# Optimization experiments

Hardware: AMD Instinct MI355X
Metric: run time of the kernel (lower is better)

The kernel has to match this reference:

```python
import jax, jax.numpy as jnp
import numpy as np

N, E, F, H, DE, C, G = 50000, 800000, 128, 128, 16, 2, 32
NEG_SLOPE = 0.2

def setup_inputs() -> dict:
    key = jax.random.key(0)
    ks = jax.random.split(key, 13)
    s = 0.05  # small init scale for weights
    return {
        "x": jax.random.normal(ks[0], (N, F), jnp.float32),
        "edge_index": jax.random.randint(ks[1], (2, E), 0, N, dtype=jnp.int32),
        "edge_attr": jax.random.normal(ks[2], (E, DE), jnp.float32),
        "batch": jnp.sort(jax.random.randint(ks[3], (N,), 0, G, dtype=jnp.int32)),
        "Wl": jax.random.normal(ks[4], (F, H), jnp.float32) * s,
        "bl": jnp.zeros((H,), jnp.float32),
        "Wr": jax.random.normal(ks[5], (F, H), jnp.float32) * s,
        "br": jnp.zeros((H,), jnp.float32),
        "We": jax.random.normal(ks[6], (DE, H), jnp.float32) * s,
        "att": jax.random.normal(ks[7], (H,), jnp.float32) * s,
        "bias_conv": jnp.zeros((H,), jnp.float32),
        "Wc": jax.random.normal(ks[8], (H, C), jnp.float32) * s,
        "bc": jnp.zeros((C,), jnp.float32),
    }

def reference(x, edge_index, edge_attr, batch, Wl, bl, Wr, br, We, att, bias_conv, Wc, bc):
    n = x.shape[0]
    src, dst = edge_index[0], edge_index[1]
    # add self loops; self-loop edge_attr = mean of incoming edge_attr (PyG fill_value='mean')
    ones_e = jnp.ones((edge_attr.shape[0],), x.dtype)
    deg = jax.ops.segment_sum(ones_e, dst, num_segments=n)
    loop_attr = jax.ops.segment_sum(edge_attr, dst, num_segments=n) / jnp.maximum(deg, 1.0)[:, None]
    idx = jnp.arange(n, dtype=src.dtype)
    src2 = jnp.concatenate([src, idx])
    dst2 = jnp.concatenate([dst, idx])
    ea2 = jnp.concatenate([edge_attr, loop_attr], axis=0)  # [E+N, DE]
    # GATv2: separate source/target transforms
    xl = x @ Wl + bl          # [N, H] (source / message features)
    xr = x @ Wr + br          # [N, H] (target features)
    e = ea2 @ We              # [E+N, H]
    m = xl[src2] + xr[dst2] + e                      # per-edge features
    logit = jax.nn.leaky_relu(m, NEG_SLOPE) @ att    # [E+N]
    # segment softmax over destination nodes (every node has a self loop)
    mx = jax.ops.segment_max(logit, dst2, num_segments=n)
    ex = jnp.exp(logit - mx[dst2])
    den = jax.ops.segment_sum(ex, dst2, num_segments=n)
    alpha = ex / den[dst2]
    out = jax.ops.segment_sum(alpha[:, None] * xl[src2], dst2, num_segments=n) + bias_conv
    h = jax.nn.relu(out)
    # global mean pool over graphs (eval mode: dropout is identity)
    cnt = jax.ops.segment_sum(jnp.ones((n,), x.dtype), batch, num_segments=G)
    pooled = jax.ops.segment_sum(h, batch, num_segments=G) / jnp.maximum(cnt, 1.0)[:, None]
    return pooled @ Wc + bc
```

## Files before the change

kernel.cpp:

```cpp
#include <hip/hip_runtime.h>

#define FDIM 128
#define HDIM 128
#define DE   16
#define GG   32
#define CAP  48
#define NPB  4
#define EA_STRIDE 20
#define NEG_SLOPE 0.2f

__device__ __forceinline__ float2 f2fma(float a, float2 b, float2 c) {
    float2 r; r.x = fmaf(a, b.x, c.x); r.y = fmaf(a, b.y, c.y); return r;
}

__global__ void k_scatter(const int* __restrict__ src, const int* __restrict__ dst,
                          int* __restrict__ cursor, int2* __restrict__ list, int E) {
    int i = blockIdx.x * blockDim.x + threadIdx.x;
    if (i < E) {
        int d = dst[i];
        int p = atomicAdd(&cursor[d], 1);
        if (p < CAP - 1) list[d * CAP + p] = make_int2(src[i], i);
    }
}

__global__ __launch_bounds__(256) void k_gemm(
    const float* __restrict__ x,
    const float* __restrict__ Wl, const float* __restrict__ bl,
    const float* __restrict__ Wr, const float* __restrict__ br,
    float* __restrict__ xl, float* __restrict__ xr, int M,
    int* __restrict__ cursor, float* __restrict__ pool, int* __restrict__ cnt)
{
    __shared__ float As[32][65];

    const int tid = threadIdx.x;
    for (int i = blockIdx.x * 256 + tid; i < M; i += gridDim.x * 256) cursor[i] = 0;
    if (blockIdx.x == 0) {
        for (int i = tid; i < GG * HDIM; i += 256) pool[i] = 0.f;
        if (tid < GG) cnt[tid] = 0;
    }
    const int r0 = blockIdx.x * 64;
    const int tx = tid & 31, ty = tid >> 5;
    float acc[8][8] = {};

    for (int kc = 0; kc < FDIM; kc += 32) {
        #pragma unroll
        for (int vv = 0; vv < 2; ++vv) {
            int v = tid + vv * 256;
            int mrow = v >> 3, kq = v & 7;
            int r = r0 + mrow; r = (r < M) ? r : (M - 1);
            float4 xv = *reinterpret_cast<const float4*>(&x[(size_t)r * FDIM + kc + kq * 4]);
            As[kq * 4 + 0][mrow] = xv.x;
            As[kq * 4 + 1][mrow] = xv.y;
            As[kq * 4 + 2][mrow] = xv.z;
            As[kq * 4 + 3][mrow] = xv.w;
        }
        __syncthreads();
        #pragma unroll
        for (int k = 0; k < 32; ++k) {
            float4 b0 = *reinterpret_cast<const float4*>(&Wl[(size_t)(kc + k) * HDIM + tx * 4]);
            float4 b1 = *reinterpret_cast<const float4*>(&Wr[(size_t)(kc + k) * HDIM + tx * 4]);
            float4 a0 = *reinterpret_cast<const float4*>(&As[k][ty * 8]);
            float4 a1 = *reinterpret_cast<const float4*>(&As[k][ty * 8 + 4]);
            float a8[8] = {a0.x, a0.y, a0.z, a0.w, a1.x, a1.y, a1.z, a1.w};
            #pragma unroll
            for (int i = 0; i < 8; ++i) {
                acc[i][0] = fmaf(a8[i], b0.x, acc[i][0]);
                acc[i][1] = fmaf(a8[i], b0.y, acc[i][1]);
                acc[i][2] = fmaf(a8[i], b0.z, acc[i][2]);
                acc[i][3] = fmaf(a8[i], b0.w, acc[i][3]);
                acc[i][4] = fmaf(a8[i], b1.x, acc[i][4]);
                acc[i][5] = fmaf(a8[i], b1.y, acc[i][5]);
                acc[i][6] = fmaf(a8[i], b1.z, acc[i][6]);
                acc[i][7] = fmaf(a8[i], b1.w, acc[i][7]);
            }
        }
        __syncthreads();
    }
    float4 bvl = *reinterpret_cast<const float4*>(&bl[tx * 4]);
    float4 bvr = *reinterpret_cast<const float4*>(&br[tx * 4]);
    #pragma unroll
    for (int i = 0; i < 8; ++i) {
        int r = r0 + ty * 8 + i;
        if (r < M) {
            float4 ol, orr;
            ol.x  = acc[i][0] + bvl.x; ol.y  = acc[i][1] + bvl.y;
            ol.z  = acc[i][2] + bvl.z; ol.w  = acc[i][3] + bvl.w;
            orr.x = acc[i][4] + bvr.x; orr.y = acc[i][5] + bvr.y;
            orr.z = acc[i][6] + bvr.z; orr.w = acc[i][7] + bvr.w;
            *reinterpret_cast<float4*>(&xl[(size_t)r * HDIM + tx * 4]) = ol;
            *reinterpret_cast<float4*>(&xr[(size_t)r * HDIM + tx * 4]) = orr;
        }
    }
}

__global__ __launch_bounds__(256, 4) void k_node(
    const float* __restrict__ xl, const float* __restrict__ xr,
    const float* __restrict__ edge_attr, const float* __restrict__ We,
    const float* __restrict__ att, const float* __restrict__ bias_conv,
    const int* __restrict__ deg, const int2* __restrict__ list,
    float* __restrict__ hN, int n0base, int N)
{
    __shared__ float ea_s[NPB][CAP][EA_STRIDE];

    const int tid  = threadIdx.x;
    const int lane = tid & 63;
    const int w    = tid >> 6;
    const int n    = n0base + blockIdx.x * NPB + w;
    if (n >= N) return;

    const float2 at2 = *reinterpret_cast<const float2*>(&att[2 * lane]);
    const float2 xr2 = *reinterpret_cast<const float2*>(&xr[(size_t)n * HDIM + 2 * lane]);
    float2 Wreg[DE];
    #pragma unroll
    for (int k = 0; k < DE; ++k)
        Wreg[k] = *reinterpret_cast<const float2*>(&We[k * HDIM + 2 * lane]);

    const int dfull  = deg[n];
    const int dcap   = dfull < (CAP - 1) ? dfull : (CAP - 1);
    const int cnt    = dcap + 1;
    const int nb     = (cnt + 7) >> 3;
    const int padcnt = nb * 8;

    if (lane < dcap) {
        int2 se = list[(size_t)n * CAP + lane];
        const float4* ep = reinterpret_cast<const float4*>(&edge_attr[(size_t)se.y * DE]);
        float4 v0 = ep[0], v1 = ep[1], v2 = ep[2], v3 = ep[3];
        float* row = &ea_s[w][lane][0];
        *reinterpret_cast<float4*>(row + 0)  = v0;
        *reinterpret_cast<float4*>(row + 4)  = v1;
        *reinterpret_cast<float4*>(row + 8)  = v2;
        *reinterpret_cast<float4*>(row + 12) = v3;
        row[16] = __int_as_float(se.x);
    } else if (lane < padcnt) {
        ea_s[w][lane][16] = __int_as_float(n);
    }
    asm volatile("s_waitcnt lgkmcnt(0)" ::: "memory");

    float2 A[8], B[8];
    int sA[8], sB[8];

    auto loadS = [&](int* s, int b) {
        #pragma unroll
        for (int jj = 0; jj < 8; ++jj)
            s[jj] = __float_as_int(ea_s[w][b * 8 + jj][16]);
    };
    auto issue = [&](float2* R, const int* s) {
        #pragma unroll
        for (int jj = 0; jj < 8; ++jj)
            R[jj] = *reinterpret_cast<const float2*>(&xl[(size_t)s[jj] * HDIM + 2 * lane]);
    };

    loadS(sA, 0);
    issue(A, sA);

    {
        const int k = lane & 15, q = lane >> 4;
        float s = 0.f;
        for (int j = q; j < dcap; j += 4) s += ea_s[w][j][k];
        s += __shfl_xor(s, 16);
        s += __shfl_xor(s, 32);
        if (q == 0) ea_s[w][dcap][k] = s / (float)(dfull > 1 ? dfull : 1);
    }
    asm volatile("s_waitcnt lgkmcnt(0)" ::: "memory");

    float m = -1e30f, d = 0.f;
    float2 o = make_float2(0.f, 0.f);

    auto compute = [&](float2* R, int b) {
        const int j0 = b * 8;
        float p[8];
        #pragma unroll
        for (int jj = 0; jj < 8; ++jj) {
            const float* ear = &ea_s[w][j0 + jj][0];
            float4 e0 = *reinterpret_cast<const float4*>(ear + 0);
            float4 e1 = *reinterpret_cast<const float4*>(ear + 4);
            float4 e2 = *reinterpret_cast<const float4*>(ear + 8);
            float4 e3 = *reinterpret_cast<const float4*>(ear + 12);
            float2 s = xr2;
            s = f2fma(e0.x, Wreg[0],  s);
            s = f2fma(e0.y, Wreg[1],  s);
            s = f2fma(e0.z, Wreg[2],  s);
            s = f2fma(e0.w, Wreg[3],  s);
            s = f2fma(e1.x, Wreg[4],  s);
            s = f2fma(e1.y, Wreg[5],  s);
            s = f2fma(e1.z, Wreg[6],  s);
            s = f2fma(e1.w, Wreg[7],  s);
            s = f2fma(e2.x, Wreg[8],  s);
            s = f2fma(e2.y, Wreg[9],  s);
            s = f2fma(e2.z, Wreg[10], s);
            s = f2fma(e2.w, Wreg[11], s);
            s = f2fma(e3.x, Wreg[12], s);
            s = f2fma(e3.y, Wreg[13], s);
            s = f2fma(e3.z, Wreg[14], s);
            s = f2fma(e3.w, Wreg[15], s);
            s.x += R[jj].x;
            s.y += R[jj].y;
            s.x = s.x > 0.f ? s.x : NEG_SLOPE * s.x;
            s.y = s.y > 0.f ? s.y : NEG_SLOPE * s.y;
            p[jj] = fmaf(s.x, at2.x, s.y * at2.y);
        }
        {
            float sd0 = (lane & 1) ? p[0] : p[4];
            float sd1 = (lane & 1) ? p[1] : p[5];
            float sd2 = (lane & 1) ? p[2] : p[6];
            float sd3 = (lane & 1) ? p[3] : p[7];
            float r0 = __shfl_xor(sd0, 1), r1 = __shfl_xor(sd1, 1);
            float r2 = __shfl_xor(sd2, 1), r3 = __shfl_xor(sd3, 1);
            p[0] = ((lane & 1) ? p[4] : p[0]) + r0;
            p[1] = ((lane & 1) ? p[5] : p[1]) + r1;
            p[2] = ((lane & 1) ? p[6] : p[2]) + r2;
            p[3] = ((lane & 1) ? p[7] : p[3]) + r3;
        }
        {
            float sd0 = (lane & 2) ? p[0] : p[2];
            float sd1 = (lane & 2) ? p[1] : p[3];
            float r0 = __shfl_xor(sd0, 2), r1 = __shfl_xor(sd1, 2);
            p[0] = ((lane & 2) ? p[2] : p[0]) + r0;
            p[1] = ((lane & 2) ? p[3] : p[1]) + r1;
        }
        {
            float sd = (lane & 4) ? p[0] : p[1];
            float r = __shfl_xor(sd, 4);
            p[0] = ((lane & 4) ? p[1] : p[0]) + r;
        }
        float t = p[0];
        t += __shfl_xor(t, 8);
        t += __shfl_xor(t, 16);
        t += __shfl_xor(t, 32);
        if (lane < 8) {
            int e = ((lane & 1) << 2) | (lane & 2) | ((lane >> 2) & 1);
            ea_s[w][e][17] = t;
        }
        asm volatile("s_waitcnt lgkmcnt(0)" ::: "memory");
        float tt[8];
        #pragma unroll
        for (int jj = 0; jj < 8; ++jj) tt[jj] = ea_s[w][jj][17];

        const int bk = cnt - j0;
        float mx = m;
        #pragma unroll
        for (int jj = 0; jj < 8; ++jj) {
            if (jj >= bk) tt[jj] = -1e30f;
            mx = fmaxf(mx, tt[jj]);
        }
        const float sc = __expf(m - mx);
        float pj[8], psum = 0.f;
        #pragma unroll
        for (int jj = 0; jj < 8; ++jj) { pj[jj] = __expf(tt[jj] - mx); psum += pj[jj]; }
        d = fmaf(d, sc, psum);
        float2 acc = make_float2(0.f, 0.f);
        #pragma unroll
        for (int jj = 0; jj < 8; ++jj) acc = f2fma(pj[jj], R[jj], acc);
        o.x = fmaf(o.x, sc, acc.x);
        o.y = fmaf(o.y, sc, acc.y);
        m = mx;
    };

    for (int b = 0; b < nb; ++b) {
        const bool odd = (b & 1) != 0;
        if (b + 1 < nb) {
            if (odd) { loadS(sA, b + 1); issue(A, sA); }
            else     { loadS(sB, b + 1); issue(B, sB); }
        }
        if (odd) compute(B, b); else compute(A, b);
    }

    const float inv = 1.f / d;
    const float2 bc2 = *reinterpret_cast<const float2*>(&bias_conv[2 * lane]);
    float2 res;
    res.x = fmaxf(fmaf(o.x, inv, bc2.x), 0.f);
    res.y = fmaxf(fmaf(o.y, inv, bc2.y), 0.f);
    *reinterpret_cast<float2*>(&hN[(size_t)n * HDIM + 2 * lane]) = res;
}

__global__ __launch_bounds__(128) void k_pool(
    const float* __restrict__ hN, const int* __restrict__ batch,
    float* __restrict__ pool, int* __restrict__ cnt, int N)
{
    const int t  = threadIdx.x;
    const int n0 = blockIdx.x * 32;
    if (n0 >= N) return;
    const int n1 = (n0 + 32 < N) ? (n0 + 32) : N;
    const int gfirst = batch[n0];
    const int glast  = batch[n1 - 1];
    if (gfirst == glast) {
        float acc = 0.f;
        #pragma unroll 8
        for (int nn = n0; nn < n1; ++nn) acc += hN[(size_t)nn * HDIM + t];
        atomicAdd(&pool[gfirst * HDIM + t], acc);
        if (t == 0) atomicAdd(&cnt[gfirst], n1 - n0);
        return;
    }
    int curg = gfirst;
    float acc = 0.f;
    int c = 0;
    for (int nn = n0; nn < n1; ++nn) {
        int g = batch[nn];
        if (g != curg) {
            atomicAdd(&pool[curg * HDIM + t], acc);
            if (t == 0) atomicAdd(&cnt[curg], c);
            acc = 0.f; c = 0; curg = g;
        }
        acc += hN[(size_t)nn * HDIM + t];
        ++c;
    }
    atomicAdd(&pool[curg * HDIM + t], acc);
    if (t == 0) atomicAdd(&cnt[curg], c);
}

__global__ void k_final(const float* __restrict__ pool, const int* __restrict__ cnt,
                        const float* __restrict__ Wc, const float* __restrict__ bc,
                        float* __restrict__ out)
{
    int t = threadIdx.x;
    if (t < GG * 2) {
        int g = t >> 1, c = t & 1;
        float inv = 1.f / (float)(cnt[g] > 1 ? cnt[g] : 1);
        float s = 0.f;
        #pragma unroll 16
        for (int h = 0; h < HDIM; ++h) s += pool[g * HDIM + h] * Wc[h * 2 + c];
        out[t] = s * inv + bc[c];
    }
}

extern "C" void kernel_launch(void* const* d_in, const int* in_sizes, int n_in,
                              void* d_out, int out_size, void* d_ws, size_t ws_size,
                              hipStream_t stream) {
    const float* x         = (const float*)d_in[0];
    const int*   ei        = (const int*)  d_in[1];
    const float* edge_attr = (const float*)d_in[2];
    const int*   batch     = (const int*)  d_in[3];
    const float* Wl        = (const float*)d_in[4];
    const float* bl        = (const float*)d_in[5];
    const float* Wr        = (const float*)d_in[6];
    const float* br        = (const float*)d_in[7];
    const float* We        = (const float*)d_in[8];
    const float* att       = (const float*)d_in[9];
    const float* bias_conv = (const float*)d_in[10];
    const float* Wc        = (const float*)d_in[11];
    const float* bc        = (const float*)d_in[12];
    float* out = (float*)d_out;

    const int N = in_sizes[0] / FDIM;
    const int E = in_sizes[1] / 2;
    const int* srcp = ei;
    const int* dstp = ei + E;

    char* ws = (char*)d_ws;
    size_t off = 0;
    auto alloc = [&](size_t bytes) { char* p = ws + off; off = (off + bytes + 255) & ~(size_t)255; return p; };
    int*   cursor = (int*)  alloc((size_t)N * 4);
    int2*  list   = (int2*) alloc((size_t)N * CAP * 8);
    float* xl     = (float*)alloc((size_t)N * HDIM * 4);
    float* xr     = (float*)alloc((size_t)N * HDIM * 4);
    float* hN     = (float*)alloc((size_t)N * HDIM * 4);
    float* pool   = (float*)alloc((size_t)GG * HDIM * 4);
    int*   cnt    = (int*)  alloc((size_t)GG * 4);

    k_gemm   <<<(N + 63) / 64, 256, 0, stream>>>(x, Wl, bl, Wr, br, xl, xr, N,
                                                 cursor, pool, cnt);
    k_scatter<<<(E + 255) / 256, 256, 0, stream>>>(srcp, dstp, cursor, list, E);

    const int per = (((N + 3) / 4 + NPB - 1) / NPB) * NPB;
    for (int q = 0; q < 4; ++q) {
        int base = q * per;
        if (base >= N) break;
        int cntq = (N - base < per) ? (N - base) : per;
        k_node<<<(cntq + NPB - 1) / NPB, 256, 0, stream>>>(
            xl, xr, edge_attr, We, att, bias_conv, cursor, list, hN, base, N);
    }

    k_pool <<<(N + 31) / 32, 128, 0, stream>>>(hN, batch, pool, cnt, N);
    k_final<<<1, 64, 0, stream>>>(pool, cnt, Wc, bc, out);
}
```

Measured before the change: 419.2 us.

## Shrink GEMM row tile with split Wl/Wr columns and launch node kernel once

The dual-projection GEMM now uses 32-row tiles. Half of the threads compute the Wl output and half the Wr output, with 32 accumulators per thread instead of 64, a smaller shared tile and a launch bound of 4 blocks per CU. This is meant to lower register pressure and raise occupancy and block count, at the cost of loading W twice as often per row. The four chunked k_node launches are merged into one full-grid launch, which removes launch gaps and tail effects.

```diff
diff --git a/kernel.cpp b/kernel.cpp
--- a/kernel.cpp
+++ b/kernel.cpp
@@ -23,14 +23,14 @@
     }
 }
 
-__global__ __launch_bounds__(256) void k_gemm(
+__global__ __launch_bounds__(256, 4) void k_gemm(
     const float* __restrict__ x,
     const float* __restrict__ Wl, const float* __restrict__ bl,
     const float* __restrict__ Wr, const float* __restrict__ br,
     float* __restrict__ xl, float* __restrict__ xr, int M,
     int* __restrict__ cursor, float* __restrict__ pool, int* __restrict__ cnt)
 {
-    __shared__ float As[32][65];
+    __shared__ float As[32][36];
 
     const int tid = threadIdx.x;
     for (int i = blockIdx.x * 256 + tid; i < M; i += gridDim.x * 256) cursor[i] = 0;
@@ -38,15 +38,19 @@
         for (int i = tid; i < GG * HDIM; i += 256) pool[i] = 0.f;
         if (tid < GG) cnt[tid] = 0;
     }
-    const int r0 = blockIdx.x * 64;
+    const int r0 = blockIdx.x * 32;
     const int tx = tid & 31, ty = tid >> 5;
-    float acc[8][8] = {};
+
+    const float* __restrict__ W    = (tx < 16) ? Wl : Wr;
+    const float* __restrict__ bias = (tx < 16) ? bl : br;
+    float* __restrict__ outp       = (tx < 16) ? xl : xr;
+    const int cb = (tx & 15) * 8;
+
+    float acc[4][8] = {};
 
     for (int kc = 0; kc < FDIM; kc += 32) {
-        #pragma unroll
-        for (int vv = 0; vv < 2; ++vv) {
-            int v = tid + vv * 256;
-            int mrow = v >> 3, kq = v & 7;
+        {
+            int mrow = tid >> 3, kq = tid & 7;
             int r = r0 + mrow; r = (r < M) ? r : (M - 1);
             float4 xv = *reinterpret_cast<const float4*>(&x[(size_t)r * FDIM + kc + kq * 4]);
             As[kq * 4 + 0][mrow] = xv.x;
@@ -55,40 +59,39 @@
             As[kq * 4 + 3][mrow] = xv.w;
         }
         __syncthreads();
-        #pragma unroll
+        #pragma unroll 4
         for (int k = 0; k < 32; ++k) {
-            float4 b0 = *reinterpret_cast<const float4*>(&Wl[(size_t)(kc + k) * HDIM + tx * 4]);
-            float4 b1 = *reinterpret_cast<const float4*>(&Wr[(size_t)(kc + k) * HDIM + tx * 4]);
-            float4 a0 = *reinterpret_cast<const float4*>(&As[k][ty * 8]);
-            float4 a1 = *reinterpret_cast<const float4*>(&As[k][ty * 8 + 4]);
-            float a8[8] = {a0.x, a0.y, a0.z, a0.w, a1.x, a1.y, a1.z, a1.w};
+            float4 b0 = *reinterpret_cast<const float4*>(&W[(size_t)(kc + k) * HDIM + cb]);
+            float4 b1 = *reinterpret_cast<const float4*>(&W[(size_t)(kc + k) * HDIM + cb + 4]);
+            float4 a  = *reinterpret_cast<const float4*>(&As[k][ty * 4]);
+            float a4[4] = {a.x, a.y, a.z, a.w};
             #pragma unroll
-            for (int i = 0; i < 8; ++i) {
-                acc[i][0] = fmaf(a8[i], b0.x, acc[i][0]);
-                acc[i][1] = fmaf(a8[i], b0.y, acc[i][1]);
-                acc[i][2] = fmaf(a8[i], b0.z, acc[i][2]);
-                acc[i][3] = fmaf(a8[i], b0.w, acc[i][3]);
-                acc[i][4] = fmaf(a8[i], b1.x, acc[i][4]);
-                acc[i][5] = fmaf(a8[i], b1.y, acc[i][5]);
-                acc[i][6] = fmaf(a8[i], b1.z, acc[i][6]);
-                acc[i][7] = fmaf(a8[i], b1.w, acc[i][7]);
+            for (int i = 0; i < 4; ++i) {
+                acc[i][0] = fmaf(a4[i], b0.x, acc[i][0]);
+                acc[i][1] = fmaf(a4[i], b0.y, acc[i][1]);
+                acc[i][2] = fmaf(a4[i], b0.z, acc[i][2]);
+                acc[i][3] = fmaf(a4[i], b0.w, acc[i][3]);
+                acc[i][4] = fmaf(a4[i], b1.x, acc[i][4]);
+                acc[i][5] = fmaf(a4[i], b1.y, acc[i][5]);
+                acc[i][6] = fmaf(a4[i], b1.z, acc[i][6]);
+                acc[i][7] = fmaf(a4[i], b1.w, acc[i][7]);
             }
         }
         __syncthreads();
     }
-    float4 bvl = *reinterpret_cast<const float4*>(&bl[tx * 4]);
-    float4 bvr = *reinterpret_cast<const float4*>(&br[tx * 4]);
+    float4 bv0 = *reinterpret_cast<const float4*>(&bias[cb]);
+    float4 bv1 = *reinterpret_cast<const float4*>(&bias[cb + 4]);
     #pragma unroll
-    for (int i = 0; i < 8; ++i) {
-        int r = r0 + ty * 8 + i;
+    for (int i = 0; i < 4; ++i) {
+        int r = r0 + ty * 4 + i;
         if (r < M) {
-            float4 ol, orr;
-            ol.x  = acc[i][0] + bvl.x; ol.y  = acc[i][1] + bvl.y;
-            ol.z  = acc[i][2] + bvl.z; ol.w  = acc[i][3] + bvl.w;
-            orr.x = acc[i][4] + bvr.x; orr.y = acc[i][5] + bvr.y;
-            orr.z = acc[i][6] + bvr.z; orr.w = acc[i][7] + bvr.w;
-            *reinterpret_cast<float4*>(&xl[(size_t)r * HDIM + tx * 4]) = ol;
-            *reinterpret_cast<float4*>(&xr[(size_t)r * HDIM + tx * 4]) = orr;
+            float4 o0, o1;
+            o0.x = acc[i][0] + bv0.x; o0.y = acc[i][1] + bv0.y;
+            o0.z = acc[i][2] + bv0.z; o0.w = acc[i][3] + bv0.w;
+            o1.x = acc[i][4] + bv1.x; o1.y = acc[i][5] + bv1.y;
+            o1.z = acc[i][6] + bv1.z; o1.w = acc[i][7] + bv1.w;
+            *reinterpret_cast<float4*>(&outp[(size_t)r * HDIM + cb])     = o0;
+            *reinterpret_cast<float4*>(&outp[(size_t)r * HDIM + cb + 4]) = o1;
         }
     }
 }
@@ -98,14 +101,14 @@
     const float* __restrict__ edge_attr, const float* __restrict__ We,
     const float* __restrict__ att, const float* __restrict__ bias_conv,
     const int* __restrict__ deg, const int2* __restrict__ list,
-    float* __restrict__ hN, int n0base, int N)
+    float* __restrict__ hN, int N)
 {
     __shared__ float ea_s[NPB][CAP][EA_STRIDE];
 
     const int tid  = threadIdx.x;
     const int lane = tid & 63;
     const int w    = tid >> 6;
-    const int n    = n0base + blockIdx.x * NPB + w;
+    const int n    = blockIdx.x * NPB + w;
     if (n >= N) return;
 
     const float2 at2 = *reinterpret_cast<const float2*>(&att[2 * lane]);
@@ -357,19 +360,11 @@
     float* pool   = (float*)alloc((size_t)GG * HDIM * 4);
     int*   cnt    = (int*)  alloc((size_t)GG * 4);
 
-    k_gemm   <<<(N + 63) / 64, 256, 0, stream>>>(x, Wl, bl, Wr, br, xl, xr, N,
+    k_gemm   <<<(N + 31) / 32, 256, 0, stream>>>(x, Wl, bl, Wr, br, xl, xr, N,
                                                  cursor, pool, cnt);
     k_scatter<<<(E + 255) / 256, 256, 0, stream>>>(srcp, dstp, cursor, list, E);
-
-    const int per = (((N + 3) / 4 + NPB - 1) / NPB) * NPB;
-    for (int q = 0; q < 4; ++q) {
-        int base = q * per;
-        if (base >= N) break;
-        int cntq = (N - base < per) ? (N - base) : per;
-        k_node<<<(cntq + NPB - 1) / NPB, 256, 0, stream>>>(
-            xl, xr, edge_attr, We, att, bias_conv, cursor, list, hN, base, N);
-    }
-
-    k_pool <<<(N + 31) / 32, 128, 0, stream>>>(hN, batch, pool, cnt, N);
-    k_final<<<1, 64, 0, stream>>>(pool, cnt, Wc, bc, out);
-}
+    k_node   <<<(N + NPB - 1) / NPB, 256, 0, stream>>>(xl, xr, edge_attr, We, att, bias_conv,
+                                                       cursor, list, hN, N);
+    k_pool   <<<(N + 31) / 32, 128, 0, stream>>>(hN, batch, pool, cnt, N);
+    k_final  <<<1, 64, 0, stream>>>(pool, cnt, Wc, bc, out);
+}
```

Result: faster. 392.1 us (-6.5%).
